# Performance work log

Measured on AMD Instinct MI355X. Metric: run time of the kernel, lower is better.

Reference implementation:

```python
import jax, jax.numpy as jnp
import numpy as np
import math

D_MODEL = 1024
N_HEADS = 16
HEAD_DIM = D_MODEL // N_HEADS  # 64
B, T = 2, 2048


def _rotate_half(x):
    x1, x2 = jnp.split(x, 2, axis=-1)
    return jnp.concatenate([-x2, x1], axis=-1)


def _rope_sin_cos(seq_len, dim, dtype=jnp.float32):
    # matches RotaryEmbedding: inv_freq over even indices, emb = [freqs, freqs]
    inv_freq = 1.0 / (10000.0 ** (jnp.arange(0, dim, 2, dtype=dtype) / dim))
    t = jnp.arange(seq_len, dtype=dtype)
    freqs = jnp.einsum('i,j->ij', t, inv_freq)          # [T, dim/2]
    emb = jnp.concatenate((freqs, freqs), axis=-1)      # [T, dim]
    sin = jnp.sin(emb)[None, :, None, :]                # [1, T, 1, dim]
    cos = jnp.cos(emb)[None, :, None, :]
    return sin, cos


def setup_inputs() -> dict:
    key = jax.random.key(0)
    k1, k2, k3 = jax.random.split(key, 3)
    x = jax.random.normal(k1, (B, T, D_MODEL), dtype=jnp.float32)
    # causal mask broadcast over batch and heads: [1, 1, T, T]
    mask = jnp.tril(jnp.ones((T, T), dtype=bool))[None, None]
    w_qkv = jax.random.normal(k2, (D_MODEL, 3 * D_MODEL), dtype=jnp.float32) / math.sqrt(D_MODEL)
    w_out = jax.random.normal(k3, (D_MODEL, D_MODEL), dtype=jnp.float32) / math.sqrt(D_MODEL)
    return {"x": x, "mask": mask, "w_qkv": w_qkv, "w_out": w_out}


def reference(x, mask, w_qkv, w_out):
    Bx, Tx, Dx = x.shape
    qkv = x @ w_qkv                                     # [B, T, 3D]
    q, k, v = jnp.split(qkv, 3, axis=-1)
    q = q.reshape(Bx, Tx, N_HEADS, HEAD_DIM)
    k = k.reshape(Bx, Tx, N_HEADS, HEAD_DIM)
    v = v.reshape(Bx, Tx, N_HEADS, HEAD_DIM)
    sin, cos = _rope_sin_cos(Tx, HEAD_DIM, x.dtype)
    q = q * cos + _rotate_half(q) * sin
    k = k * cos + _rotate_half(k) * sin
    scores = jnp.einsum('bthd,bThd->bhtT', q, k) / math.sqrt(HEAD_DIM)
    scores = jnp.where(mask, scores, -1e10)
    probs = jax.nn.softmax(scores, axis=-1)             # [B, H, T, T]
    out = jnp.einsum('bhtT,bThd->bthd', probs, v)
    out = out.reshape(Bx, Tx, Dx)
    return out @ w_out
```

## Files before the change

### kernel.cpp

```cpp
#include <hip/hip_runtime.h>
#include <math.h>

typedef unsigned short u16;
typedef __attribute__((ext_vector_type(8))) short short8;
typedef __attribute__((ext_vector_type(4))) float f32x4;

__device__ __forceinline__ u16 f2bf(float f) {
  unsigned int u = __float_as_uint(f);
  u += 0x7fffu + ((u >> 16) & 1u);
  return (u16)(u >> 16);
}
__device__ __forceinline__ float bf2f(u16 h) {
  return __uint_as_float(((unsigned int)h) << 16);
}

__device__ __forceinline__ f32x4 mfma16(short8 a, short8 b, f32x4 c) {
  return __builtin_amdgcn_mfma_f32_16x16x32_bf16(a, b, c, 0, 0, 0);
}

#define NEG_BIG (-1e30f)

__global__ __launch_bounds__(256) void detect_dtype3(const u16* __restrict__ a,
                                                     const u16* __restrict__ bb,
                                                     const u16* __restrict__ c,
                                                     int* __restrict__ flags) {
  const u16* x = (blockIdx.x == 0) ? a : (blockIdx.x == 1) ? bb : c;
  __shared__ int cnt;
  if (threadIdx.x == 0) cnt = 0;
  __syncthreads();
  int my = 0;
  for (int i = threadIdx.x; i < 4096; i += 256) {
    float v = bf2f(x[2 * i]);
    float av = fabsf(v);
    if (v == 0.0f || (av >= 1e-4f && av <= 100.0f)) my++;
  }
  atomicAdd(&cnt, my);
  __syncthreads();
  if (threadIdx.x == 0) flags[blockIdx.x] = (cnt > 2458) ? 1 : 0;
}

__global__ __launch_bounds__(256) void transpose_to_bf16(const void* __restrict__ in,
                                                         u16* __restrict__ out,
                                                         int R, int C,
                                                         const int* __restrict__ flag) {
  __shared__ float tile[64][68];
  bool isbf = (*flag != 0);
  int tc = blockIdx.x * 64, tr = blockIdx.y * 64;
  int tid = threadIdx.x;
  int r = tid >> 3, cg = (tid & 7) << 3;
#pragma unroll
  for (int p = 0; p < 2; ++p) {
    int row = r + p * 32;
    if (isbf) {
      short8 v = *(const short8*)((const u16*)in + (size_t)(tr + row) * C + tc + cg);
#pragma unroll
      for (int u = 0; u < 8; ++u) tile[row][cg + u] = bf2f((u16)v[u]);
    } else {
      const float* inf = (const float*)in + (size_t)(tr + row) * C + tc + cg;
#pragma unroll
      for (int u = 0; u < 8; ++u) tile[row][cg + u] = inf[u];
    }
  }
  __syncthreads();
#pragma unroll
  for (int p = 0; p < 2; ++p) {
    int orow = r + p * 32;
    short8 v;
#pragma unroll
    for (int u = 0; u < 8; ++u) v[u] = (short)f2bf(tile[cg + u][orow]);
    *(short8*)(out + (size_t)(tc + orow) * R + tr + cg) = v;
  }
}

__global__ __launch_bounds__(256) void convert_x(const void* __restrict__ xin,
                                                 u16* __restrict__ xb,
                                                 const int* __restrict__ flag) {
  bool isbf = (*flag != 0);
  int base = (blockIdx.x * 256 + threadIdx.x) * 8;
  if (isbf) {
    *(short8*)(xb + base) = *(const short8*)((const u16*)xin + base);
  } else {
    const float* xf = (const float*)xin;
    f32x4 x0 = *(const f32x4*)(xf + base);
    f32x4 x1 = *(const f32x4*)(xf + base + 4);
    short8 o;
#pragma unroll
    for (int u = 0; u < 4; ++u) { o[u] = (short)f2bf(x0[u]); o[u + 4] = (short)f2bf(x1[u]); }
    *(short8*)(xb + base) = o;
  }
}

__device__ __forceinline__ void qkv_epilogue(f32x4 acc[4][4], int bm, int bn,
                                             int wm, int wn, int quad, int lane15,
                                             u16* Qo, u16* Ko, u16* VTo) {
  int nbase = bn + wn * 64;
  int h = (nbase & 1023) >> 6;
  float invf0 = __expf(-(float)lane15 * 0.28782313662425575f);
  float invf1 = __expf(-(float)(lane15 + 16) * 0.28782313662425575f);
  bool isQ = nbase < 1024;
#pragma unroll
  for (int i = 0; i < 4; ++i) {
#pragma unroll
    for (int r = 0; r < 4; ++r) {
      int m = bm + wm * 64 + i * 16 + quad * 4 + r;
      int b = m >> 11, t = m & 2047;
      float v0 = acc[i][0][r], v1 = acc[i][1][r], v2 = acc[i][2][r], v3 = acc[i][3][r];
      if (nbase < 2048) {
        float s0, c0, s1, c1;
        sincosf((float)t * invf0, &s0, &c0);
        sincosf((float)t * invf1, &s1, &c1);
        float o0 = v0 * c0 - v2 * s0;
        float o1 = v1 * c1 - v3 * s1;
        float o2 = v2 * c0 + v0 * s0;
        float o3 = v3 * c1 + v1 * s1;
        u16* dst = isQ ? Qo : Ko;
        size_t base = ((size_t)(b * 16 + h) * 2048 + t) * 64;
        dst[base + lane15] = f2bf(o0);
        dst[base + 16 + lane15] = f2bf(o1);
        dst[base + 32 + lane15] = f2bf(o2);
        dst[base + 48 + lane15] = f2bf(o3);
      } else {
        size_t vb = (size_t)(b * 16 + h) * 64;
        VTo[(vb + lane15) * 2048 + t] = f2bf(v0);
        VTo[(vb + 16 + lane15) * 2048 + t] = f2bf(v1);
        VTo[(vb + 32 + lane15) * 2048 + t] = f2bf(v2);
        VTo[(vb + 48 + lane15) * 2048 + t] = f2bf(v3);
      }
    }
  }
}

__global__ __launch_bounds__(256) void gemm_qkv_fast(const u16* __restrict__ X,
                                                     const u16* __restrict__ WT,
                                                     u16* __restrict__ Qo,
                                                     u16* __restrict__ Ko,
                                                     u16* __restrict__ VTo) {
  const int K = 1024;
  __shared__ u16 lA[128 * 32];
  __shared__ u16 lB[128 * 32];
  int tid = threadIdx.x;
  int wave = tid >> 6, lane = tid & 63;
  int lane15 = lane & 15, quad = lane >> 4;
  int wm = wave >> 1, wn = wave & 1;
  int bm = blockIdx.x * 128, bn = blockIdx.y * 128;
  f32x4 acc[4][4] = {};
  for (int k0 = 0; k0 < K; k0 += 32) {
    __syncthreads();
#pragma unroll
    for (int p = 0; p < 2; ++p) {
      int g = p * 4 + wave;
      int f = g * 64 + lane;
      int row = f >> 2, cc = (f & 3) << 3;
      __builtin_amdgcn_global_load_lds(
          (const __attribute__((address_space(1))) unsigned int*)(X + (size_t)(bm + row) * K + k0 + cc),
          (__attribute__((address_space(3))) unsigned int*)(lA + g * 512), 16, 0, 0);
      __builtin_amdgcn_global_load_lds(
          (const __attribute__((address_space(1))) unsigned int*)(WT + (size_t)(bn + row) * K + k0 + cc),
          (__attribute__((address_space(3))) unsigned int*)(lB + g * 512), 16, 0, 0);
    }
    __syncthreads();
    short8 af[4], bf[4];
#pragma unroll
    for (int i = 0; i < 4; ++i)
      af[i] = *(const short8*)(lA + (wm * 64 + i * 16 + lane15) * 32 + quad * 8);
#pragma unroll
    for (int j = 0; j < 4; ++j)
      bf[j] = *(const short8*)(lB + (wn * 64 + j * 16 + lane15) * 32 + quad * 8);
#pragma unroll
    for (int i = 0; i < 4; ++i)
#pragma unroll
      for (int j = 0; j < 4; ++j)
        acc[i][j] = mfma16(af[i], bf[j], acc[i][j]);
  }
  qkv_epilogue(acc, bm, bn, wm, wn, quad, lane15, Qo, Ko, VTo);
}

__global__ __launch_bounds__(256) void gemm_qkv_rope(const void* __restrict__ Xv,
                                                     const u16* __restrict__ WT,
                                                     u16* __restrict__ Qo,
                                                     u16* __restrict__ Ko,
                                                     u16* __restrict__ VTo,
                                                     const int* __restrict__ flag) {
  const int K = 1024;
  __shared__ u16 lA[128 * 40];
  __shared__ u16 lB[128 * 40];
  bool isbf = (*flag != 0);
  int tid = threadIdx.x;
  int wave = tid >> 6, lane = tid & 63;
  int lane15 = lane & 15, quad = lane >> 4;
  int wm = wave >> 1, wn = wave & 1;
  int bm = blockIdx.x * 128, bn = blockIdx.y * 128;
  int sr = tid >> 2, scg = (tid & 3) << 3;
  f32x4 acc[4][4] = {};
  for (int k0 = 0; k0 < K; k0 += 32) {
    __syncthreads();
#pragma unroll
    for (int p = 0; p < 2; ++p) {
      int row = sr + p * 64;
      if (isbf) {
        *(short8*)(lA + row * 40 + scg) =
            *(const short8*)((const u16*)Xv + (size_t)(bm + row) * K + k0 + scg);
      } else {
        const float* xf = (const float*)Xv + (size_t)(bm + row) * K + k0 + scg;
        f32x4 x0 = *(const f32x4*)(xf);
        f32x4 x1 = *(const f32x4*)(xf + 4);
        short8 o;
#pragma unroll
        for (int u = 0; u < 4; ++u) { o[u] = (short)f2bf(x0[u]); o[u + 4] = (short)f2bf(x1[u]); }
        *(short8*)(lA + row * 40 + scg) = o;
      }
      *(short8*)(lB + row * 40 + scg) = *(const short8*)(WT + (size_t)(bn + row) * K + k0 + scg);
    }
    __syncthreads();
    short8 af[4], bf[4];
#pragma unroll
    for (int i = 0; i < 4; ++i)
      af[i] = *(const short8*)(lA + (wm * 64 + i * 16 + lane15) * 40 + quad * 8);
#pragma unroll
    for (int j = 0; j < 4; ++j)
      bf[j] = *(const short8*)(lB + (wn * 64 + j * 16 + lane15) * 40 + quad * 8);
#pragma unroll
    for (int i = 0; i < 4; ++i)
#pragma unroll
      for (int j = 0; j < 4; ++j)
        acc[i][j] = mfma16(af[i], bf[j], acc[i][j]);
  }
  qkv_epilogue(acc, bm, bn, wm, wn, quad, lane15, Qo, Ko, VTo);
}

__device__ __forceinline__ short8 lds_frag(const u16* buf, int row, int chunk) {
  int s = chunk ^ (row & 7);
  return *(const short8*)(buf + row * 64 + s * 8);
}

__device__ __forceinline__ void stage_tile(const u16* gK, const u16* gV,
                                           u16* lK, u16* lV, int wave, int lane) {
#pragma unroll
  for (int p = 0; p < 2; ++p) {
    int f = (p * 4 + wave) * 64 + lane;
    int r = f >> 3;
    int c = (f & 7) ^ (r & 7);
    __builtin_amdgcn_global_load_lds(
        (const __attribute__((address_space(1))) unsigned int*)(gK + (size_t)r * 64 + c * 8),
        (__attribute__((address_space(3))) unsigned int*)(lK + (p * 4 + wave) * 512),
        16, 0, 0);
    __builtin_amdgcn_global_load_lds(
        (const __attribute__((address_space(1))) unsigned int*)(gV + (size_t)r * 2048 + c * 8),
        (__attribute__((address_space(3))) unsigned int*)(lV + (p * 4 + wave) * 512),
        16, 0, 0);
  }
}

__global__ __launch_bounds__(256, 4) void attn_fused(const u16* __restrict__ Q,
                                                     const u16* __restrict__ K,
                                                     const u16* __restrict__ VT,
                                                     u16* __restrict__ Ao) {
  int bx = blockIdx.x;
  int bh = bx & 31;
  int kp = bx >> 5;
  int m = kp & 7, n = kp >> 3;
  int qt = (n == 0) ? m : (n == 1) ? (15 - m) : (n == 2) ? (16 + m) : (31 - m);
  int b = bh >> 4, h = bh & 15;
  int tid = threadIdx.x, wave = tid >> 6, lane = tid & 63;
  int lane15 = lane & 15, quad = lane >> 4;
  int q0 = qt * 64 + wave * 16;
  const u16* Qb = Q + (size_t)bh * 2048 * 64;
  const u16* Kb = K + (size_t)bh * 2048 * 64;
  const u16* Vb = VT + (size_t)bh * 64 * 2048;

  __shared__ u16 Kl[2][64 * 64];
  __shared__ u16 Vl[2][64 * 64];
  __shared__ u16 lP[4][16 * 64];
  u16* myP = lP[wave];

  short8 qf0 = *(const short8*)(Qb + (size_t)(q0 + lane15) * 64 + quad * 8);
  short8 qf1 = *(const short8*)(Qb + (size_t)(q0 + lane15) * 64 + 32 + quad * 8);

  f32x4 Ov[4] = {};
  float tsum[4] = {0.f, 0.f, 0.f, 0.f};

  int ntiles = qt + 1;
  stage_tile(Kb, Vb, Kl[0], Vl[0], wave, lane);

  for (int kt = 0; kt < ntiles; ++kt) {
    int kbase = kt * 64;
    int cur = kt & 1;
    __syncthreads();
    if (kt + 1 < ntiles)
      stage_tile(Kb + (size_t)(kbase + 64) * 64, Vb + kbase + 64,
                 Kl[cur ^ 1], Vl[cur ^ 1], wave, lane);

    f32x4 S[4];
#pragma unroll
    for (int j = 0; j < 4; ++j) {
      short8 k0 = lds_frag(Kl[cur], j * 16 + lane15, quad);
      short8 k1 = lds_frag(Kl[cur], j * 16 + lane15, 4 + quad);
      f32x4 z = {};
      z = mfma16(qf0, k0, z);
      z = mfma16(qf1, k1, z);
      S[j] = z;
    }
    if (kt == qt) {
#pragma unroll
      for (int j = 0; j < 4; ++j) {
        int kpos = kbase + j * 16 + lane15;
#pragma unroll
        for (int r = 0; r < 4; ++r)
          if (kpos > q0 + quad * 4 + r) S[j][r] = NEG_BIG;
      }
    }
#pragma unroll
    for (int j = 0; j < 4; ++j)
#pragma unroll
      for (int r = 0; r < 4; ++r) {
        float p = __expf(fmaf(S[j][r], 0.125f, -8.0f));
        S[j][r] = p;
        tsum[r] += p;
      }
#pragma unroll
    for (int j = 0; j < 4; ++j)
#pragma unroll
      for (int r = 0; r < 4; ++r) {
        int lrow = quad * 4 + r;
        int slot = (j * 2 + (lane15 >> 3)) ^ (lrow & 7);
        myP[lrow * 64 + slot * 8 + (lane15 & 7)] = f2bf(S[j][r]);
      }
    asm volatile("s_waitcnt lgkmcnt(0)" ::: "memory");
    short8 pa0 = *(const short8*)(myP + lane15 * 64 + ((quad) ^ (lane15 & 7)) * 8);
    short8 pa1 = *(const short8*)(myP + lane15 * 64 + ((4 + quad) ^ (lane15 & 7)) * 8);
#pragma unroll
    for (int j = 0; j < 4; ++j) {
      short8 v0 = lds_frag(Vl[cur], j * 16 + lane15, quad);
      short8 v1 = lds_frag(Vl[cur], j * 16 + lane15, 4 + quad);
      Ov[j] = mfma16(pa0, v0, Ov[j]);
      Ov[j] = mfma16(pa1, v1, Ov[j]);
    }
  }
  float rl[4];
#pragma unroll
  for (int r = 0; r < 4; ++r) {
    float v = tsum[r];
    v += __shfl_xor(v, 1);
    v += __shfl_xor(v, 2);
    v += __shfl_xor(v, 4);
    v += __shfl_xor(v, 8);
    rl[r] = 1.f / v;
  }
#pragma unroll
  for (int j = 0; j < 4; ++j)
#pragma unroll
    for (int r = 0; r < 4; ++r) {
      int t = q0 + quad * 4 + r;
      Ao[(size_t)(b * 2048 + t) * 1024 + h * 64 + j * 16 + lane15] =
          f2bf(Ov[j][r] * rl[r]);
    }
}

__global__ __launch_bounds__(256) void gemm_out(const u16* __restrict__ A,
                                                const u16* __restrict__ WT,
                                                float* __restrict__ out) {
  const int K = 1024;
  __shared__ u16 lA[128 * 32];
  __shared__ u16 lB[128 * 32];
  int tid = threadIdx.x;
  int wave = tid >> 6, lane = tid & 63;
  int lane15 = lane & 15, quad = lane >> 4;
  int wm = wave >> 1, wn = wave & 1;
  int bm = blockIdx.x * 128, bn = blockIdx.y * 128;
  f32x4 acc[4][4] = {};
  for (int k0 = 0; k0 < K; k0 += 32) {
    __syncthreads();
#pragma unroll
    for (int p = 0; p < 2; ++p) {
      int g = p * 4 + wave;
      int f = g * 64 + lane;
      int row = f >> 2, cc = (f & 3) << 3;
      __builtin_amdgcn_global_load_lds(
          (const __attribute__((address_space(1))) unsigned int*)(A + (size_t)(bm + row) * K + k0 + cc),
          (__attribute__((address_space(3))) unsigned int*)(lA + g * 512), 16, 0, 0);
      __builtin_amdgcn_global_load_lds(
          (const __attribute__((address_space(1))) unsigned int*)(WT + (size_t)(bn + row) * K + k0 + cc),
          (__attribute__((address_space(3))) unsigned int*)(lB + g * 512), 16, 0, 0);
    }
    __syncthreads();
    short8 af[4], bf[4];
#pragma unroll
    for (int i = 0; i < 4; ++i)
      af[i] = *(const short8*)(lA + (wm * 64 + i * 16 + lane15) * 32 + quad * 8);
#pragma unroll
    for (int j = 0; j < 4; ++j)
      bf[j] = *(const short8*)(lB + (wn * 64 + j * 16 + lane15) * 32 + quad * 8);
#pragma unroll
    for (int i = 0; i < 4; ++i)
#pragma unroll
      for (int j = 0; j < 4; ++j)
        acc[i][j] = mfma16(af[i], bf[j], acc[i][j]);
  }
#pragma unroll
  for (int i = 0; i < 4; ++i)
#pragma unroll
    for (int r = 0; r < 4; ++r) {
      int m = bm + wm * 64 + i * 16 + quad * 4 + r;
      size_t rowo = (size_t)m * 1024 + bn + wn * 64 + lane15;
      out[rowo] = acc[i][0][r];
      out[rowo + 16] = acc[i][1][r];
      out[rowo + 32] = acc[i][2][r];
      out[rowo + 48] = acc[i][3][r];
    }
}

__global__ void ws_sentinel(float* out, float val) {
  if (threadIdx.x == 0) out[1] = val;
}

extern "C" void kernel_launch(void* const* d_in, const int* in_sizes, int n_in,
                              void* d_out, int out_size, void* d_ws, size_t ws_size,
                              hipStream_t stream) {
  (void)out_size;
  const void* x = nullptr;
  const void* w_qkv = nullptr;
  const void* w_out = nullptr;
  for (int i = 0; i < n_in; ++i) {
    if (in_sizes[i] == 4194304 && !x) x = d_in[i];
    else if (in_sizes[i] == 3145728 && !w_qkv) w_qkv = d_in[i];
    else if (in_sizes[i] == 1048576 && !w_out) w_out = d_in[i];
  }
  float* out = (float*)d_out;

  const size_t REQ_EL = 32 + 4194304 + 1048576 + 3 * 4194304;
  const size_t REQUIRED = REQ_EL * 2;
  const size_t REQ_FAST = (REQ_EL + 4194304) * 2;
  if (ws_size < REQUIRED) {
    ws_sentinel<<<1, 64, 0, stream>>>(out, 1.0e6f + 1000.0f * (float)(ws_size >> 20));
    return;
  }
  int* flags = (int*)d_ws;
  u16* base = (u16*)d_ws + 32;
  u16* wqkvT = base;
  u16* attnw = base;
  u16* woutT = base + 4194304;
  u16* Qw = woutT + 1048576;
  u16* Kw = Qw + 4194304;
  u16* VTw = Kw + 4194304;
  u16* xb = VTw + 4194304;

  detect_dtype3<<<3, 256, 0, stream>>>((const u16*)x, (const u16*)w_qkv,
                                       (const u16*)w_out, flags);
  transpose_to_bf16<<<dim3(48, 16), 256, 0, stream>>>(w_qkv, wqkvT, 1024, 3072, flags + 1);
  transpose_to_bf16<<<dim3(16, 16), 256, 0, stream>>>(w_out, woutT, 1024, 1024, flags + 2);
  if (ws_size >= REQ_FAST) {
    convert_x<<<2048, 256, 0, stream>>>(x, xb, flags + 0);
    gemm_qkv_fast<<<dim3(32, 24), 256, 0, stream>>>(xb, wqkvT, Qw, Kw, VTw);
  } else {
    gemm_qkv_rope<<<dim3(32, 24), 256, 0, stream>>>(x, wqkvT, Qw, Kw, VTw, flags + 0);
  }
  attn_fused<<<1024, 256, 0, stream>>>(Qw, Kw, VTw, attnw);
  gemm_out<<<dim3(32, 8), 256, 0, stream>>>(attnw, woutT, out);
}
```

Baseline: 208.6 us.

## Precompute RoPE table, stage QKV epilogue in LDS, merge prep kernels, retile out-GEMM

Merges the two weight-transpose launches into one prep kernel, which also writes a precomputed RoPE cos/sin table. The QKV GEMM epilogue now reads that table instead of calling sincosf per element. It stages its bf16 results in shared memory so Q/K and the transposed V are written as coalesced 16-byte stores. The output GEMM uses 64-row tiles, doubling the grid for better occupancy across CUs. The cost is extra workspace for the table, an added barrier plus LDS round trip in the epilogue, and less B-tile reuse per block in the output GEMM.

```diff
diff --git a/kernel.cpp b/kernel.cpp
--- a/kernel.cpp
+++ b/kernel.cpp
@@ -39,14 +39,32 @@
   if (threadIdx.x == 0) flags[blockIdx.x] = (cnt > 2458) ? 1 : 0;
 }
 
-__global__ __launch_bounds__(256) void transpose_to_bf16(const void* __restrict__ in,
-                                                         u16* __restrict__ out,
-                                                         int R, int C,
-                                                         const int* __restrict__ flag) {
+__global__ __launch_bounds__(256) void prep_kernel(const void* __restrict__ wqkv,
+                                                   const void* __restrict__ wout,
+                                                   u16* __restrict__ wqkvT,
+                                                   u16* __restrict__ woutT,
+                                                   float2* __restrict__ tab,
+                                                   const int* __restrict__ flags) {
+  int z = blockIdx.z;
+  int tid = threadIdx.x;
+  if (z == 2) {
+    if (blockIdx.x >= 16 || blockIdx.y >= 16) return;
+    int idx = (blockIdx.y * 16 + blockIdx.x) * 256 + tid;
+    int t = idx >> 5, d = idx & 31;
+    float invf = expf(-(float)d * 0.28782313662425575f);
+    float s, c;
+    sincosf((float)t * invf, &s, &c);
+    tab[idx] = make_float2(c, s);
+    return;
+  }
+  const void* in = (z == 0) ? wqkv : wout;
+  u16* out = (z == 0) ? wqkvT : woutT;
+  int C = (z == 0) ? 3072 : 1024;
+  const int R = 1024;
+  bool isbf = (flags[z + 1] != 0);
+  if (z == 1 && blockIdx.x >= 16) return;
   __shared__ float tile[64][68];
-  bool isbf = (*flag != 0);
   int tc = blockIdx.x * 64, tr = blockIdx.y * 64;
-  int tid = threadIdx.x;
   int r = tid >> 3, cg = (tid & 7) << 3;
 #pragma unroll
   for (int p = 0; p < 2; ++p) {
@@ -90,54 +108,71 @@
   }
 }
 
-__device__ __forceinline__ void qkv_epilogue(f32x4 acc[4][4], int bm, int bn,
-                                             int wm, int wn, int quad, int lane15,
-                                             u16* Qo, u16* Ko, u16* VTo) {
+__device__ __forceinline__ void qkv_epilogue2(f32x4 acc[4][4], int bm, int bn,
+                                              int wm, int wn, int quad, int lane15,
+                                              int lane, const float2* __restrict__ tab,
+                                              u16* Qo, u16* Ko, u16* VTo, u16* eplds) {
   int nbase = bn + wn * 64;
   int h = (nbase & 1023) >> 6;
-  float invf0 = __expf(-(float)lane15 * 0.28782313662425575f);
-  float invf1 = __expf(-(float)(lane15 + 16) * 0.28782313662425575f);
-  bool isQ = nbase < 1024;
-#pragma unroll
-  for (int i = 0; i < 4; ++i) {
-#pragma unroll
-    for (int r = 0; r < 4; ++r) {
-      int m = bm + wm * 64 + i * 16 + quad * 4 + r;
-      int b = m >> 11, t = m & 2047;
-      float v0 = acc[i][0][r], v1 = acc[i][1][r], v2 = acc[i][2][r], v3 = acc[i][3][r];
-      if (nbase < 2048) {
-        float s0, c0, s1, c1;
-        sincosf((float)t * invf0, &s0, &c0);
-        sincosf((float)t * invf1, &s1, &c1);
-        float o0 = v0 * c0 - v2 * s0;
-        float o1 = v1 * c1 - v3 * s1;
-        float o2 = v2 * c0 + v0 * s0;
-        float o3 = v3 * c1 + v1 * s1;
-        u16* dst = isQ ? Qo : Ko;
-        size_t base = ((size_t)(b * 16 + h) * 2048 + t) * 64;
-        dst[base + lane15] = f2bf(o0);
-        dst[base + 16 + lane15] = f2bf(o1);
-        dst[base + 32 + lane15] = f2bf(o2);
-        dst[base + 48 + lane15] = f2bf(o3);
-      } else {
-        size_t vb = (size_t)(b * 16 + h) * 64;
-        VTo[(vb + lane15) * 2048 + t] = f2bf(v0);
-        VTo[(vb + 16 + lane15) * 2048 + t] = f2bf(v1);
-        VTo[(vb + 32 + lane15) * 2048 + t] = f2bf(v2);
-        VTo[(vb + 48 + lane15) * 2048 + t] = f2bf(v3);
+  bool isV = nbase >= 2048;
+  if (!isV) {
+#pragma unroll
+    for (int i = 0; i < 4; ++i) {
+#pragma unroll
+      for (int r = 0; r < 4; ++r) {
+        int mloc = i * 16 + quad * 4 + r;
+        int t = (bm + wm * 64 + mloc) & 2047;
+        float2 cs0 = tab[t * 32 + lane15];
+        float2 cs1 = tab[t * 32 + 16 + lane15];
+        float v0 = acc[i][0][r], v1 = acc[i][1][r], v2 = acc[i][2][r], v3 = acc[i][3][r];
+        eplds[mloc * 68 + lane15]      = f2bf(v0 * cs0.x - v2 * cs0.y);
+        eplds[mloc * 68 + 16 + lane15] = f2bf(v1 * cs1.x - v3 * cs1.y);
+        eplds[mloc * 68 + 32 + lane15] = f2bf(v2 * cs0.x + v0 * cs0.y);
+        eplds[mloc * 68 + 48 + lane15] = f2bf(v3 * cs1.x + v1 * cs1.y);
       }
+    }
+    asm volatile("s_waitcnt lgkmcnt(0)" ::: "memory");
+    u16* dst = (nbase < 1024) ? Qo : Ko;
+#pragma unroll
+    for (int p = 0; p < 8; ++p) {
+      int f = p * 64 + lane;
+      int mr = f >> 3, nc = f & 7;
+      int g = bm + wm * 64 + mr;
+      int bI = g >> 11, tI = g & 2047;
+      short8 val = *(const short8*)(eplds + mr * 68 + nc * 8);
+      *(short8*)(dst + ((size_t)(bI * 16 + h) * 2048 + tI) * 64 + nc * 8) = val;
+    }
+  } else {
+#pragma unroll
+    for (int i = 0; i < 4; ++i)
+#pragma unroll
+      for (int j = 0; j < 4; ++j)
+#pragma unroll
+        for (int r = 0; r < 4; ++r)
+          eplds[(j * 16 + lane15) * 68 + i * 16 + quad * 4 + r] = f2bf(acc[i][j][r]);
+    asm volatile("s_waitcnt lgkmcnt(0)" ::: "memory");
+    int g0 = bm + wm * 64;
+    int bI = g0 >> 11, t0 = g0 & 2047;
+#pragma unroll
+    for (int p = 0; p < 8; ++p) {
+      int f = p * 64 + lane;
+      int dr = f >> 3, tc = f & 7;
+      short8 val = *(const short8*)(eplds + dr * 68 + tc * 8);
+      *(short8*)(VTo + ((size_t)(bI * 16 + h) * 64 + dr) * 2048 + t0 + tc * 8) = val;
     }
   }
 }
 
 __global__ __launch_bounds__(256) void gemm_qkv_fast(const u16* __restrict__ X,
                                                      const u16* __restrict__ WT,
+                                                     const float2* __restrict__ tab,
                                                      u16* __restrict__ Qo,
                                                      u16* __restrict__ Ko,
                                                      u16* __restrict__ VTo) {
   const int K = 1024;
-  __shared__ u16 lA[128 * 32];
-  __shared__ u16 lB[128 * 32];
+  __shared__ u16 buf[4 * 4352];
+  u16* lA = buf;
+  u16* lB = buf + 4096;
   int tid = threadIdx.x;
   int wave = tid >> 6, lane = tid & 63;
   int lane15 = lane & 15, quad = lane >> 4;
@@ -172,18 +207,22 @@
       for (int j = 0; j < 4; ++j)
         acc[i][j] = mfma16(af[i], bf[j], acc[i][j]);
   }
-  qkv_epilogue(acc, bm, bn, wm, wn, quad, lane15, Qo, Ko, VTo);
+  __syncthreads();
+  qkv_epilogue2(acc, bm, bn, wm, wn, quad, lane15, lane, tab, Qo, Ko, VTo,
+                buf + wave * 4352);
 }
 
 __global__ __launch_bounds__(256) void gemm_qkv_rope(const void* __restrict__ Xv,
                                                      const u16* __restrict__ WT,
+                                                     const float2* __restrict__ tab,
                                                      u16* __restrict__ Qo,
                                                      u16* __restrict__ Ko,
                                                      u16* __restrict__ VTo,
                                                      const int* __restrict__ flag) {
   const int K = 1024;
-  __shared__ u16 lA[128 * 40];
-  __shared__ u16 lB[128 * 40];
+  __shared__ u16 buf[4 * 4352];
+  u16* lA = buf;
+  u16* lB = buf + 5120;
   bool isbf = (*flag != 0);
   int tid = threadIdx.x;
   int wave = tid >> 6, lane = tid & 63;
@@ -225,7 +264,9 @@
       for (int j = 0; j < 4; ++j)
         acc[i][j] = mfma16(af[i], bf[j], acc[i][j]);
   }
-  qkv_epilogue(acc, bm, bn, wm, wn, quad, lane15, Qo, Ko, VTo);
+  __syncthreads();
+  qkv_epilogue2(acc, bm, bn, wm, wn, quad, lane15, lane, tab, Qo, Ko, VTo,
+                buf + wave * 4352);
 }
 
 __device__ __forceinline__ short8 lds_frag(const u16* buf, int row, int chunk) {
@@ -360,47 +401,56 @@
                                                 const u16* __restrict__ WT,
                                                 float* __restrict__ out) {
   const int K = 1024;
-  __shared__ u16 lA[128 * 32];
+  __shared__ u16 lA[64 * 32];
   __shared__ u16 lB[128 * 32];
   int tid = threadIdx.x;
   int wave = tid >> 6, lane = tid & 63;
   int lane15 = lane & 15, quad = lane >> 4;
   int wm = wave >> 1, wn = wave & 1;
-  int bm = blockIdx.x * 128, bn = blockIdx.y * 128;
-  f32x4 acc[4][4] = {};
+  int bm = blockIdx.x * 64, bn = blockIdx.y * 128;
+  f32x4 acc[2][4] = {};
   for (int k0 = 0; k0 < K; k0 += 32) {
     __syncthreads();
 #pragma unroll
-    for (int p = 0; p < 2; ++p) {
-      int g = p * 4 + wave;
-      int f = g * 64 + lane;
-      int row = f >> 2, cc = (f & 3) << 3;
-      __builtin_amdgcn_global_load_lds(
-          (const __attribute__((address_space(1))) unsigned int*)(A + (size_t)(bm + row) * K + k0 + cc),
-          (__attribute__((address_space(3))) unsigned int*)(lA + g * 512), 16, 0, 0);
-      __builtin_amdgcn_global_load_lds(
-          (const __attribute__((address_space(1))) unsigned int*)(WT + (size_t)(bn + row) * K + k0 + cc),
-          (__attribute__((address_space(3))) unsigned int*)(lB + g * 512), 16, 0, 0);
-    }
-    __syncthreads();
-    short8 af[4], bf[4];
-#pragma unroll
-    for (int i = 0; i < 4; ++i)
-      af[i] = *(const short8*)(lA + (wm * 64 + i * 16 + lane15) * 32 + quad * 8);
+    for (int q = 0; q < 3; ++q) {
+      int blk = wave * 3 + q;
+      int f, row, cc;
+      if (blk < 4) {
+        f = blk * 64 + lane;
+        row = f >> 2;
+        cc = (f & 3) << 3;
+        __builtin_amdgcn_global_load_lds(
+            (const __attribute__((address_space(1))) unsigned int*)(A + (size_t)(bm + row) * K + k0 + cc),
+            (__attribute__((address_space(3))) unsigned int*)(lA + blk * 512), 16, 0, 0);
+      } else {
+        int bblk = blk - 4;
+        f = bblk * 64 + lane;
+        row = f >> 2;
+        cc = (f & 3) << 3;
+        __builtin_amdgcn_global_load_lds(
+            (const __attribute__((address_space(1))) unsigned int*)(WT + (size_t)(bn + row) * K + k0 + cc),
+            (__attribute__((address_space(3))) unsigned int*)(lB + bblk * 512), 16, 0, 0);
+      }
+    }
+    __syncthreads();
+    short8 af[2], bf[4];
+#pragma unroll
+    for (int i = 0; i < 2; ++i)
+      af[i] = *(const short8*)(lA + (wm * 32 + i * 16 + lane15) * 32 + quad * 8);
 #pragma unroll
     for (int j = 0; j < 4; ++j)
       bf[j] = *(const short8*)(lB + (wn * 64 + j * 16 + lane15) * 32 + quad * 8);
 #pragma unroll
-    for (int i = 0; i < 4; ++i)
+    for (int i = 0; i < 2; ++i)
 #pragma unroll
       for (int j = 0; j < 4; ++j)
         acc[i][j] = mfma16(af[i], bf[j], acc[i][j]);
   }
 #pragma unroll
-  for (int i = 0; i < 4; ++i)
+  for (int i = 0; i < 2; ++i)
 #pragma unroll
     for (int r = 0; r < 4; ++r) {
-      int m = bm + wm * 64 + i * 16 + quad * 4 + r;
+      int m = bm + wm * 32 + i * 16 + quad * 4 + r;
       size_t rowo = (size_t)m * 1024 + bn + wn * 64 + lane15;
       out[rowo] = acc[i][0][r];
       out[rowo + 16] = acc[i][1][r];
@@ -427,10 +477,10 @@
   }
   float* out = (float*)d_out;
 
-  const size_t REQ_EL = 32 + 4194304 + 1048576 + 3 * 4194304;
-  const size_t REQUIRED = REQ_EL * 2;
-  const size_t REQ_FAST = (REQ_EL + 4194304) * 2;
-  if (ws_size < REQUIRED) {
+  const size_t EL_B = 32 + 4194304 + 1048576 + 3 * 4194304 + 262144;
+  const size_t REQ_B = EL_B * 2;
+  const size_t REQ_A = (EL_B + 4194304) * 2;
+  if (ws_size < REQ_B) {
     ws_sentinel<<<1, 64, 0, stream>>>(out, 1.0e6f + 1000.0f * (float)(ws_size >> 20));
     return;
   }
@@ -442,18 +492,18 @@
   u16* Qw = woutT + 1048576;
   u16* Kw = Qw + 4194304;
   u16* VTw = Kw + 4194304;
-  u16* xb = VTw + 4194304;
+  float2* tab = (float2*)(VTw + 4194304);
+  u16* xb = VTw + 4194304 + 262144;
 
   detect_dtype3<<<3, 256, 0, stream>>>((const u16*)x, (const u16*)w_qkv,
                                        (const u16*)w_out, flags);
-  transpose_to_bf16<<<dim3(48, 16), 256, 0, stream>>>(w_qkv, wqkvT, 1024, 3072, flags + 1);
-  transpose_to_bf16<<<dim3(16, 16), 256, 0, stream>>>(w_out, woutT, 1024, 1024, flags + 2);
-  if (ws_size >= REQ_FAST) {
+  prep_kernel<<<dim3(48, 16, 3), 256, 0, stream>>>(w_qkv, w_out, wqkvT, woutT, tab, flags);
+  if (ws_size >= REQ_A) {
     convert_x<<<2048, 256, 0, stream>>>(x, xb, flags + 0);
-    gemm_qkv_fast<<<dim3(32, 24), 256, 0, stream>>>(xb, wqkvT, Qw, Kw, VTw);
+    gemm_qkv_fast<<<dim3(32, 24), 256, 0, stream>>>(xb, wqkvT, tab, Qw, Kw, VTw);
   } else {
-    gemm_qkv_rope<<<dim3(32, 24), 256, 0, stream>>>(x, wqkvT, Qw, Kw, VTw, flags + 0);
+    gemm_qkv_rope<<<dim3(32, 24), 256, 0, stream>>>(x, wqkvT, tab, Qw, Kw, VTw, flags + 0);
   }
   attn_fused<<<1024, 256, 0, stream>>>(Qw, Kw, VTw, attnw);
-  gemm_out<<<dim3(32, 8), 256, 0, stream>>>(attnw, woutT, out);
-}
+  gemm_out<<<dim3(64, 8), 256, 0, stream>>>(attnw, woutT, out);
+}
```

Measured after the change: 207.5 us. Within noise of the previous version (-0.5%).
